# Performance work log

Measured on AMD Instinct MI355X. Metric: run time of the kernel, lower is better.

## Reference

```python
import jax, jax.numpy as jnp
import numpy as np

NUM_RGAP = NUM_SGAP = NUM_PCOUNT = NUM_PRCOUNT = 100
EMB = 256
B, S = 128, 500


def setup_inputs() -> dict:
    key = jax.random.key(0)
    k = jax.random.split(key, 8)
    return {
        "rgap": jax.random.randint(k[0], (B, S), 0, NUM_RGAP),
        "sgap": jax.random.randint(k[1], (B, S), 0, NUM_SGAP),
        "pcount": jax.random.randint(k[2], (B, S), 0, NUM_PCOUNT),
        "prcount": jax.random.randint(k[3], (B, S), 0, NUM_PRCOUNT),
        # Tables are weight.T of the bias-free Linears: out = one_hot(idx) @ W.T = W.T[idx]
        "Wr": jax.random.normal(k[4], (NUM_RGAP, EMB), dtype=jnp.float32) * 0.02,
        "Ws": jax.random.normal(k[5], (NUM_SGAP, EMB), dtype=jnp.float32) * 0.02,
        "Wp": jax.random.normal(k[6], (NUM_PCOUNT, EMB), dtype=jnp.float32) * 0.02,
        "Wpr": jax.random.normal(k[7], (NUM_PRCOUNT, EMB), dtype=jnp.float32) * 0.02,
    }


def reference(rgap, sgap, pcount, prcount, Wr, Ws, Wp, Wpr):
    # one_hot(idx) @ W.T is exactly a row gather from W.T; no dense one-hot needed.
    return (
        Wr[rgap],    # [B, S, EMB]
        Ws[sgap],
        Wp[pcount],
        Wpr[prcount],
    )
```

## Files before the change

### kernel.cpp

```cpp
#include <hip/hip_runtime.h>
#include <hip/hip_bf16.h>


typedef float f32x4 __attribute__((ext_vector_type(4)));

#define ROWS        64000
#define V4_ROW      64
#define V4_TAB      (ROWS * V4_ROW)
#define NTHREADS    512000
#define ITERS       8

__global__ __launch_bounds__(256) void gather4_kernel(
    const int* __restrict__ i0, const int* __restrict__ i1,
    const int* __restrict__ i2, const int* __restrict__ i3,
    const f32x4* __restrict__ w0, const f32x4* __restrict__ w1,
    const f32x4* __restrict__ w2, const f32x4* __restrict__ w3,
    f32x4* __restrict__ out)
{
    const int* idx[4] = {i0, i1, i2, i3};
    const f32x4* w[4] = {w0, w1, w2, w3};

    const int tid = blockIdx.x * 256 + threadIdx.x;

#pragma unroll
    for (int k = 0; k < ITERS; ++k) {
        const int j = tid + k * NTHREADS;
        const int r = j >> 6;
        const int l = j & 63;
#pragma unroll
        for (int t = 0; t < 4; ++t) {
            const int id = idx[t][r];
            const f32x4 v = w[t][id * V4_ROW + l];
            __builtin_nontemporal_store(v, &out[(long)t * V4_TAB + j]);
        }
    }
}

extern "C" void kernel_launch(void* const* d_in, const int* in_sizes, int n_in,
                              void* d_out, int out_size, void* d_ws, size_t ws_size,
                              hipStream_t stream) {
    const int* rgap    = (const int*)d_in[0];
    const int* sgap    = (const int*)d_in[1];
    const int* pcount  = (const int*)d_in[2];
    const int* prcount = (const int*)d_in[3];
    const f32x4* Wr  = (const f32x4*)d_in[4];
    const f32x4* Ws  = (const f32x4*)d_in[5];
    const f32x4* Wp  = (const f32x4*)d_in[6];
    const f32x4* Wpr = (const f32x4*)d_in[7];
    f32x4* out = (f32x4*)d_out;

    gather4_kernel<<<2000, 256, 0, stream>>>(
        rgap, sgap, pcount, prcount, Wr, Ws, Wp, Wpr, out);
}
```

Measured before the change: 51.48 us.

## Stage embedding tables in LDS and assign one table-chunk per block

Each block copies one full 100-row table plus its chunk of indices into shared memory, then writes its output slice by reading rows from LDS. Grid becomes 256 blocks of 512 threads, each covering 1000 rows of one table. This aims to remove global gather reads, but it adds a preload phase before any stores, runs one block per CU with lower occupancy, and drops nontemporal stores on a write-bound workload.

```diff
diff --git a/kernel.cpp b/kernel.cpp
--- a/kernel.cpp
+++ b/kernel.cpp
@@ -4,35 +4,45 @@
 
 typedef float f32x4 __attribute__((ext_vector_type(4)));
 
-#define ROWS        64000
+#define ROWS_TAB    64000
 #define V4_ROW      64
-#define V4_TAB      (ROWS * V4_ROW)
-#define NTHREADS    512000
-#define ITERS       8
+#define V4_TAB      (ROWS_TAB * V4_ROW)
+#define TAB_V4      6400
+#define BLK_TABLES  64
+#define ROWS_BLK    1000
+#define V4_BLK      64000
+#define THREADS     512
+#define MAIN_ITERS  125
 
-__global__ __launch_bounds__(256) void gather4_kernel(
+__global__ __launch_bounds__(THREADS, 1) void gather_lds_kernel(
     const int* __restrict__ i0, const int* __restrict__ i1,
     const int* __restrict__ i2, const int* __restrict__ i3,
     const f32x4* __restrict__ w0, const f32x4* __restrict__ w1,
     const f32x4* __restrict__ w2, const f32x4* __restrict__ w3,
     f32x4* __restrict__ out)
 {
-    const int* idx[4] = {i0, i1, i2, i3};
-    const f32x4* w[4] = {w0, w1, w2, w3};
+    __shared__ f32x4 tab[TAB_V4];
+    __shared__ int   ridx[ROWS_BLK];
 
-    const int tid = blockIdx.x * 256 + threadIdx.x;
+    const int b   = blockIdx.x;
+    const int t   = b >> 6;
+    const int c   = b & 63;
+    const int tid = threadIdx.x;
 
-#pragma unroll
-    for (int k = 0; k < ITERS; ++k) {
-        const int j = tid + k * NTHREADS;
-        const int r = j >> 6;
-        const int l = j & 63;
-#pragma unroll
-        for (int t = 0; t < 4; ++t) {
-            const int id = idx[t][r];
-            const f32x4 v = w[t][id * V4_ROW + l];
-            __builtin_nontemporal_store(v, &out[(long)t * V4_TAB + j]);
-        }
+    const int*   idx = (t == 0) ? i0 : (t == 1) ? i1 : (t == 2) ? i2 : i3;
+    const f32x4* w   = (t == 0) ? w0 : (t == 1) ? w1 : (t == 2) ? w2 : w3;
+
+    for (int i = tid; i < TAB_V4; i += THREADS) tab[i] = w[i];
+    for (int i = tid; i < ROWS_BLK; i += THREADS) ridx[i] = idx[c * ROWS_BLK + i];
+    __syncthreads();
+
+    f32x4* o = out + (long)t * V4_TAB + (long)c * V4_BLK;
+#pragma unroll 5
+    for (int it = 0; it < MAIN_ITERS; ++it) {
+        const int jl = it * THREADS + tid;
+        const int r  = jl >> 6;
+        const int l  = jl & 63;
+        o[jl] = tab[ridx[r] * V4_ROW + l];
     }
 }
 
@@ -49,6 +59,6 @@
     const f32x4* Wpr = (const f32x4*)d_in[7];
     f32x4* out = (f32x4*)d_out;
 
-    gather4_kernel<<<2000, 256, 0, stream>>>(
+    gather_lds_kernel<<<256, THREADS, 0, stream>>>(
         rgap, sgap, pcount, prcount, Wr, Ws, Wp, Wpr, out);
 }
```

After: 47.43 us. 1.09x faster.
